# Kernel optimization log

Measured on AMD Instinct MI355X. Metric: run time of the kernel, lower is better.

Reference implementation:

```python
import jax, jax.numpy as jnp
import numpy as np
from jax import lax

DIM = 192
HEADS = 4
K = 3
PAD = 1


def conv2d(x, w, groups=1, pad=0):
    # x: [B,C,H,W], w: [O, C//groups, kh, kw]
    return lax.conv_general_dilated(
        x, w, window_strides=(1, 1), padding=[(pad, pad), (pad, pad)],
        dimension_numbers=("NCHW", "OIHW", "NCHW"), feature_group_count=groups)


def setup_inputs() -> dict:
    key = jax.random.key(0)
    ks = jax.random.split(key, 8)
    b, c, h, w = 2, DIM, 256, 256
    x = jax.random.normal(ks[0], (b, c, h, w), dtype=jnp.float32)
    y = jax.random.normal(ks[1], (b, c, h, w), dtype=jnp.float32)
    s = 0.05
    qk_w = jax.random.normal(ks[2], (2 * DIM, DIM, 1, 1), dtype=jnp.float32) * s
    qk_dw_w = jax.random.normal(ks[3], (2 * DIM, 1, K, K), dtype=jnp.float32) * s  # depthwise, groups=2*dim
    v_w = jax.random.normal(ks[4], (DIM, DIM, 1, 1), dtype=jnp.float32) * s
    v_dw_w = jax.random.normal(ks[5], (DIM, DIM, K, K), dtype=jnp.float32) * s    # NOTE: not grouped in source
    proj_w = jax.random.normal(ks[6], (DIM, DIM, 1, 1), dtype=jnp.float32) * s
    temperature = jnp.ones((HEADS, 1, 1), dtype=jnp.float32)
    return {"x": x, "y": y, "qk_w": qk_w, "qk_dw_w": qk_dw_w, "v_w": v_w,
            "v_dw_w": v_dw_w, "proj_w": proj_w, "temperature": temperature}


def reference(x, y, qk_w, qk_dw_w, v_w, v_dw_w, proj_w, temperature):
    b, c, h, w = x.shape
    hd = c // HEADS  # channels per head
    qk = conv2d(conv2d(x, qk_w), qk_dw_w, groups=2 * DIM, pad=PAD)  # [b, 2c, h, w]
    q, k = jnp.split(qk, 2, axis=1)
    v = conv2d(conv2d(y, v_w), v_dw_w, pad=PAD)  # full conv (groups=1), per source

    def to_heads(t):
        return t.reshape(b, HEADS, hd, h * w)  # b head c (hw)

    q, k, v = to_heads(q), to_heads(k), to_heads(v)
    # L2 normalize along spatial (last) axis, eps matches torch F.normalize (1e-12)
    q = q / jnp.maximum(jnp.linalg.norm(q, axis=-1, keepdims=True), 1e-12)
    k = k / jnp.maximum(jnp.linalg.norm(k, axis=-1, keepdims=True), 1e-12)
    attn = jnp.einsum("bhcn,bhdn->bhcd", q, k) * temperature  # [b, head, c, c]
    attn = jax.nn.softmax(attn, axis=-1)
    out = jnp.einsum("bhcd,bhdn->bhcn", attn, v)
    out = out.reshape(b, c, h, w)
    return conv2d(out, proj_w)
```

## Files before the change

### kernel.cpp

```cpp
#include <hip/hip_runtime.h>
#include <hip/hip_bf16.h>

#define NPIX 65536
#define CDIM 192
#define C2   384
#define HEADS 4
#define HD   48
#define PROW 258
#define XTROWS (PROW * PROW)

typedef float f32x4 __attribute__((ext_vector_type(4)));
typedef short short8 __attribute__((ext_vector_type(8)));

__device__ __forceinline__ unsigned short f2bf(float x) {
  union { float f; unsigned u; } v; v.f = x;
  unsigned r = v.u + 0x7fff + ((v.u >> 16) & 1);
  return (unsigned short)(r >> 16);
}
__device__ __forceinline__ float bf2f(unsigned short x) {
  union { unsigned u; float f; } v; v.u = ((unsigned)x) << 16;
  return v.f;
}
__device__ __forceinline__ int f4(int r) { return (r ^ (r >> 2)) & 3; }

__device__ __forceinline__ void gload_lds16(const void* g, void* l) {
  __builtin_amdgcn_global_load_lds(
      (const __attribute__((address_space(1))) unsigned int*)g,
      (__attribute__((address_space(3))) unsigned int*)l, 16, 0, 0);
}

__global__ __launch_bounds__(256) void castw_kernel(
    const float* __restrict__ qkw, const float* __restrict__ vw,
    unsigned short* __restrict__ wqk, unsigned short* __restrict__ wv) {
  int i = blockIdx.x * 256 + threadIdx.x;
  if (i < C2 * CDIM) wqk[i] = f2bf(qkw[i]);
  if (i < CDIM * CDIM) wv[i] = f2bf(vw[i]);
}

__global__ __launch_bounds__(512) void qk_mfma_kernel(
    const float* __restrict__ X, const unsigned short* __restrict__ W,
    unsigned short* __restrict__ Out) {
  const int px0 = blockIdx.x * 128;
  __shared__ __align__(16) short smem[17408];
  short* sA = smem;
  short* sB = smem + 12288;
  const int t = threadIdx.x;
  const int lane = t & 63;
  const int wid = t >> 6;
  const int cp = t & 15;
  const int pg = t >> 4;
  const int l15 = lane & 15;
  const int l4 = lane >> 4;

  f32x4 acc[3][8];
#pragma unroll
  for (int mi = 0; mi < 3; ++mi)
#pragma unroll
    for (int ni = 0; ni < 8; ++ni) acc[mi][ni] = (f32x4){0.f, 0.f, 0.f, 0.f};

  for (int k0 = 0; k0 < CDIM; k0 += 32) {
#pragma unroll
    for (int i = 0; i < 3; ++i) {
      int e = i * 512 + t;
      int oc = e >> 2, kg = e & 3;
      gload_lds16(W + (size_t)oc * CDIM + k0 + (kg ^ f4(oc)) * 8,
                  (char*)sA + ((size_t)i * 512 + (t & ~63)) * 16);
    }
    {
      const float* xp = X + (size_t)(k0 + 2 * cp) * NPIX + px0 + 4 * pg;
      float4 a = *(const float4*)xp;
      float4 b = *(const float4*)(xp + NPIX);
      float av[4] = {a.x, a.y, a.z, a.w};
      float bv[4] = {b.x, b.y, b.z, b.w};
#pragma unroll
      for (int i = 0; i < 4; ++i) {
        unsigned d = (unsigned)f2bf(av[i]) | ((unsigned)f2bf(bv[i]) << 16);
        *(unsigned*)&sB[(4 * pg + i) * 40 + 2 * cp] = d;
      }
    }
    asm volatile("s_waitcnt vmcnt(0)");
    __syncthreads();
    short8 af[3], bf[8];
#pragma unroll
    for (int mi = 0; mi < 3; ++mi) {
      int row = wid * 48 + mi * 16 + l15;
      af[mi] = *(const short8*)&sA[row * 32 + (l4 ^ f4(row)) * 8];
    }
#pragma unroll
    for (int ni = 0; ni < 8; ++ni)
      bf[ni] = *(const short8*)&sB[(ni * 16 + l15) * 40 + l4 * 8];
#pragma unroll
    for (int mi = 0; mi < 3; ++mi)
#pragma unroll
      for (int ni = 0; ni < 8; ++ni)
        acc[mi][ni] = __builtin_amdgcn_mfma_f32_16x16x32_bf16(
            af[mi], bf[ni], acc[mi][ni], 0, 0, 0);
    __syncthreads();
  }
  __syncthreads();
  short* zone = smem + wid * 2176;
#pragma unroll
  for (int mi = 0; mi < 3; ++mi) {
#pragma unroll
    for (int ni = 0; ni < 8; ++ni)
#pragma unroll
      for (int rg = 0; rg < 4; ++rg)
        zone[(l4 * 4 + rg) * 136 + ni * 16 + l15] =
            (short)f2bf(acc[mi][ni][rg]);
    asm volatile("s_waitcnt lgkmcnt(0)" ::: "memory");
    __builtin_amdgcn_sched_barrier(0);
#pragma unroll
    for (int it = 0; it < 4; ++it) {
      int e = it * 64 + lane;
      int ol = e >> 4, pxg = e & 15;
      short8 vv = *(const short8*)&zone[ol * 136 + pxg * 8];
      *(short8*)&Out[(size_t)(wid * 48 + mi * 16 + ol) * NPIX + px0 + pxg * 8] = vv;
    }
    asm volatile("s_waitcnt lgkmcnt(0)" ::: "memory");
    __builtin_amdgcn_sched_barrier(0);
  }
}

__global__ __launch_bounds__(256) void v_mfma_kernel(
    const float* __restrict__ Y, const unsigned short* __restrict__ W,
    unsigned short* __restrict__ Xt) {
  const int px0 = blockIdx.x * 64;
  const int h = px0 >> 8;
  const int w0 = px0 & 255;
  __shared__ short sX[64 * 40];
  __shared__ short sW[CDIM * 32];
  __shared__ short sZ[4 * 16 * 200];
  const int t = threadIdx.x;
  const int lane = t & 63;
  const int wid = t >> 6;
  const int cp = t & 15;
  const int pg = t >> 4;
  const int l15 = lane & 15;
  const int l4 = lane >> 4;

  f32x4 acc[12];
#pragma unroll
  for (int ni = 0; ni < 12; ++ni) acc[ni] = (f32x4){0.f, 0.f, 0.f, 0.f};

  for (int k0 = 0; k0 < CDIM; k0 += 32) {
#pragma unroll
    for (int i = 0; i < 3; ++i) {
      int e = i * 256 + t;
      int oc = e >> 2, kg = e & 3;
      gload_lds16(W + (size_t)oc * CDIM + k0 + (kg ^ f4(oc)) * 8,
                  (char*)sW + ((size_t)i * 256 + (t & ~63)) * 16);
    }
    {
      const float* xp = Y + (size_t)(k0 + 2 * cp) * NPIX + px0 + 4 * pg;
      float4 a = *(const float4*)xp;
      float4 b = *(const float4*)(xp + NPIX);
      float av[4] = {a.x, a.y, a.z, a.w};
      float bv[4] = {b.x, b.y, b.z, b.w};
#pragma unroll
      for (int i = 0; i < 4; ++i) {
        unsigned d = (unsigned)f2bf(av[i]) | ((unsigned)f2bf(bv[i]) << 16);
        *(unsigned*)&sX[(4 * pg + i) * 40 + 2 * cp] = d;
      }
    }
    asm volatile("s_waitcnt vmcnt(0)");
    __syncthreads();
    short8 af = *(const short8*)&sX[(wid * 16 + l15) * 40 + l4 * 8];
    short8 bf[12];
#pragma unroll
    for (int ni = 0; ni < 12; ++ni) {
      int row = ni * 16 + l15;
      bf[ni] = *(const short8*)&sW[row * 32 + (l4 ^ f4(row)) * 8];
    }
#pragma unroll
    for (int ni = 0; ni < 12; ++ni)
      acc[ni] = __builtin_amdgcn_mfma_f32_16x16x32_bf16(af, bf[ni], acc[ni],
                                                        0, 0, 0);
    __syncthreads();
  }
  short* zone = sZ + wid * (16 * 200);
#pragma unroll
  for (int ni = 0; ni < 12; ++ni)
#pragma unroll
    for (int rg = 0; rg < 4; ++rg)
      zone[(l4 * 4 + rg) * 200 + ni * 16 + l15] = (short)f2bf(acc[ni][rg]);
  asm volatile("s_waitcnt lgkmcnt(0)" ::: "memory");
  __builtin_amdgcn_sched_barrier(0);
#pragma unroll
  for (int it = 0; it < 6; ++it) {
    int e = it * 64 + lane;
    int pl = e / 24, cg = e % 24;
    short8 vv = *(const short8*)&zone[pl * 200 + cg * 8];
    size_t xrow = (size_t)(h + 1) * PROW + (w0 + wid * 16 + pl + 1);
    *(short8*)&Xt[xrow * CDIM + cg * 8] = vv;
  }
}

__global__ __launch_bounds__(128) void border_zero_kernel(
    unsigned short* __restrict__ Xt) {
  int pos = blockIdx.x;
  size_t row;
  if (pos < 258) row = pos;
  else if (pos < 516) row = (size_t)257 * PROW + (pos - 258);
  else { int i = pos - 516; row = (size_t)(1 + (i >> 1)) * PROW + ((i & 1) ? 257 : 0); }
  unsigned* p = (unsigned*)(Xt + row * CDIM);
  if (threadIdx.x < 96) p[threadIdx.x] = 0;
}

__global__ __launch_bounds__(256) void dwgram_kernel(
    const unsigned short* __restrict__ qkb, const float* __restrict__ dw,
    float* __restrict__ gpart_b, float* __restrict__ ssp_b) {
  const int head = blockIdx.y;
  const int blk = blockIdx.x;
  const int t = threadIdx.x;
  const int lane = t & 63;
  const int wid = t >> 6;

  __shared__ __align__(16) char smem[38400];
  short* zone = (short*)smem + wid * (96 * 40);

  const int qrow0 = HD * head, krow0 = CDIM + HD * head;
  const int p0 = (lane & 1) * 16;
  const int c0 = (lane >> 1) * 3;

  float wr[3][9];
#pragma unroll
  for (int j = 0; j < 3; ++j) {
    int ch = c0 + j;
    int srow = (ch < HD) ? (qrow0 + ch) : (krow0 + ch - HD);
#pragma unroll
    for (int i = 0; i < 9; ++i) wr[j][i] = dw[srow * 9 + i];
  }

  f32x4 acc[3][3];
#pragma unroll
  for (int mi = 0; mi < 3; ++mi)
#pragma unroll
    for (int nj = 0; nj < 3; ++nj) acc[mi][nj] = (f32x4){0.f, 0.f, 0.f, 0.f};
  float ss[3] = {0.f, 0.f, 0.f};

  const int pxbase = blk * 512 + wid * 128;
  for (int s = 0; s < 4; ++s) {
    const int px0 = pxbase + s * 32;
    const int hr = px0 >> 8;
    const int col0 = px0 & 255;
    const int cl = col0 + p0;
#pragma unroll
    for (int j = 0; j < 3; ++j) {
      int ch = c0 + j;
      int srow = (ch < HD) ? (qrow0 + ch) : (krow0 + ch - HD);
      const unsigned short* ip = qkb + (size_t)srow * NPIX;
      float win[3][18];
#pragma unroll
      for (int r = 0; r < 3; ++r) {
        int ir = hr - 1 + r;
        if ((unsigned)ir < 256u) {
          const unsigned short* rp = ip + ir * 256 + cl;
          short8 v0 = *(const short8*)rp;
          short8 v1 = *(const short8*)(rp + 8);
#pragma unroll
          for (int q = 0; q < 8; ++q) {
            win[r][1 + q] = bf2f((unsigned short)v0[q]);
            win[r][9 + q] = bf2f((unsigned short)v1[q]);
          }
          win[r][0]  = (cl > 0)        ? bf2f(rp[-1]) : 0.f;
          win[r][17] = (cl + 16 < 256) ? bf2f(rp[16]) : 0.f;
        } else {
#pragma unroll
          for (int q = 0; q < 18; ++q) win[r][q] = 0.f;
        }
      }
      unsigned pk[8];
#pragma unroll
      for (int p = 0; p < 16; ++p) {
        float sacc = 0.f;
#pragma unroll
        for (int r = 0; r < 3; ++r)
#pragma unroll
          for (int c = 0; c < 3; ++c) sacc += wr[j][r * 3 + c] * win[r][p + c];
        ss[j] += sacc * sacc;
        unsigned short bb = f2bf(sacc);
        if (p & 1) pk[p >> 1] |= ((unsigned)bb << 16);
        else       pk[p >> 1] = bb;
      }
      unsigned* zp = (unsigned*)&zone[ch * 40 + p0];
#pragma unroll
      for (int q = 0; q < 8; ++q) zp[q] = pk[q];
    }
    asm volatile("s_waitcnt lgkmcnt(0)" ::: "memory");
    __builtin_amdgcn_sched_barrier(0);
    short8 qf[3], kf[3];
#pragma unroll
    for (int mi = 0; mi < 3; ++mi)
      qf[mi] = *(const short8*)&zone[(mi * 16 + (lane & 15)) * 40 +
                                     (lane >> 4) * 8];
#pragma unroll
    for (int nj = 0; nj < 3; ++nj)
      kf[nj] = *(const short8*)&zone[(HD + nj * 16 + (lane & 15)) * 40 +
                                     (lane >> 4) * 8];
#pragma unroll
    for (int mi = 0; mi < 3; ++mi)
#pragma unroll
      for (int nj = 0; nj < 3; ++nj)
        acc[mi][nj] = __builtin_amdgcn_mfma_f32_16x16x32_bf16(
            qf[mi], kf[nj], acc[mi][nj], 0, 0, 0);
    asm volatile("s_waitcnt lgkmcnt(0)" ::: "memory");
    __builtin_amdgcn_sched_barrier(0);
  }
  __syncthreads();
  float* red   = (float*)smem;
  float* ssred = (float*)(smem + 36864);
#pragma unroll
  for (int mi = 0; mi < 3; ++mi)
#pragma unroll
    for (int nj = 0; nj < 3; ++nj) {
      int kj = nj * 16 + (lane & 15);
#pragma unroll
      for (int rg = 0; rg < 4; ++rg) {
        int qi = mi * 16 + (lane >> 4) * 4 + rg;
        red[wid * 2304 + qi * HD + kj] = acc[mi][nj][rg];
      }
    }
#pragma unroll
  for (int j = 0; j < 3; ++j) {
    float sj = ss[j] + __shfl_xor(ss[j], 1);
    if ((lane & 1) == 0) ssred[wid * 96 + c0 + j] = sj;
  }
  __syncthreads();
  float* gp = gpart_b + (size_t)(head * 128 + blk) * (HD * HD);
  for (int e = t; e < HD * HD; e += 256)
    gp[e] = red[e] + red[2304 + e] + red[4608 + e] + red[6912 + e];
  if (t < 96)
    ssp_b[(size_t)(head * 128 + blk) * 96 + t] =
        ssred[t] + ssred[96 + t] + ssred[192 + t] + ssred[288 + t];
}

__global__ __launch_bounds__(128) void normred_kernel(
    const float* __restrict__ ssp, float* __restrict__ norms) {
  int idx = blockIdx.x;
  int bh = idx / 96, ch = idx % 96;
  int l = threadIdx.x;
  float s = ssp[((size_t)bh * 128 + l) * 96 + ch];
#pragma unroll
  for (int off = 32; off; off >>= 1) s += __shfl_down(s, off);
  __shared__ float red[2];
  if ((l & 63) == 0) red[l >> 6] = s;
  __syncthreads();
  if (l == 0) {
    int b = bh >> 2, hh = bh & 3;
    int g = b * C2 + (ch < HD ? hh * HD + ch : CDIM + hh * HD + ch - HD);
    norms[g] = sqrtf(red[0] + red[1]);
  }
}

__global__ __launch_bounds__(256) void gramred_kernel(
    const float* __restrict__ part, float* __restrict__ logits) {
  int ij = blockIdx.x * 256 + threadIdx.x;
  int bh = blockIdx.y;
  if (ij >= HD * HD) return;
  const float* pp = part + (size_t)bh * 128 * (HD * HD);
  float s = 0.f;
  for (int sp = 0; sp < 128; ++sp) s += pp[(size_t)sp * (HD * HD) + ij];
  logits[(size_t)bh * (HD * HD) + ij] = s;
}

__global__ __launch_bounds__(64) void softmax_kernel(
    float* __restrict__ logits, const float* __restrict__ norms,
    const float* __restrict__ temperature) {
  int hh = blockIdx.x, b = blockIdx.y;
  int i = threadIdx.x;
  if (i >= HD) return;
  const float eps = 1e-12f;
  float temp = temperature[hh];
  float nq = fmaxf(norms[b * C2 + HD * hh + i], eps);
  float* row = logits + (((size_t)b * HEADS + hh) * HD + i) * HD;
  float vals[48];
  float mx = -1e30f;
#pragma unroll
  for (int j = 0; j < HD; ++j) {
    float nk = fmaxf(norms[b * C2 + CDIM + HD * hh + j], eps);
    float v = row[j] / (nq * nk) * temp;
    vals[j] = v;
    mx = fmaxf(mx, v);
  }
  float sum = 0.f;
#pragma unroll
  for (int j = 0; j < HD; ++j) {
    vals[j] = expf(vals[j] - mx);
    sum += vals[j];
  }
  float inv = 1.f / sum;
#pragma unroll
  for (int j = 0; j < HD; ++j) row[j] = vals[j] * inv;
}

__global__ __launch_bounds__(256) void buildM_kernel(
    const float* __restrict__ attn, const float* __restrict__ projw,
    float* __restrict__ M) {
  int idx = blockIdx.x * 256 + threadIdx.x;
  if (idx >= 2 * CDIM * CDIM) return;
  int d = idx % CDIM;
  int oc = (idx / CDIM) % CDIM;
  int b = idx / (CDIM * CDIM);
  int hh = d / HD, dd = d % HD;
  const float* arow = attn + ((size_t)b * HEADS + hh) * HD * HD;
  float s = 0.f;
#pragma unroll
  for (int c = 0; c < HD; ++c)
    s += projw[oc * CDIM + HD * hh + c] * arow[c * HD + dd];
  M[idx] = s;
}

__global__ __launch_bounds__(256) void wtrans_kernel(
    const float* __restrict__ M, const float* __restrict__ Wv,
    unsigned short* __restrict__ Wb) {
  const int ocb = blockIdx.x * 4;
  const int ec0 = blockIdx.y * 432;
  const int b = blockIdx.z;
  __shared__ float sM[4][CDIM];
  for (int i = threadIdx.x; i < 4 * CDIM; i += 256)
    sM[i / CDIM][i % CDIM] =
        M[((size_t)b * CDIM + ocb + i / CDIM) * CDIM + (i % CDIM)];
  __syncthreads();
  for (int e = ec0 + threadIdx.x; e < ec0 + 432; e += 256) {
    float a0 = 0.f, a1 = 0.f, a2 = 0.f, a3 = 0.f;
#pragma unroll 4
    for (int d = 0; d < CDIM; ++d) {
      float wv = Wv[(size_t)d * (CDIM * 9) + e];
      a0 += sM[0][d] * wv; a1 += sM[1][d] * wv;
      a2 += sM[2][d] * wv; a3 += sM[3][d] * wv;
    }
    int ic = e / 9, tap = e % 9;
    size_t base = (((size_t)b * 9 + tap) * CDIM) * CDIM + ic;
    Wb[base + (size_t)(ocb + 0) * CDIM] = f2bf(a0);
    Wb[base + (size_t)(ocb + 1) * CDIM] = f2bf(a1);
    Wb[base + (size_t)(ocb + 2) * CDIM] = f2bf(a2);
    Wb[base + (size_t)(ocb + 3) * CDIM] = f2bf(a3);
  }
}

__global__ __launch_bounds__(256) void conv3x3_mfma_kernel(
    const unsigned short* __restrict__ Xt,
    const unsigned short* __restrict__ Wb,
    float* __restrict__ out) {
  const int d = blockIdx.x;
  const int xcd = d & 7;
  const int j = d >> 3;
  const int h = xcd * 32 + j / 3;
  const int oc0 = (j % 3) * 64;

  __shared__ __align__(16) short sA[2][3 * 64 * 32];
  __shared__ __align__(16) short sB[2][260 * 32];

  const int t = threadIdx.x;
  const int lane = t & 63;
  const int wid = t >> 6;
  const int l15 = lane & 15;
  const int l4 = lane >> 4;

  f32x4 acc[4][4];
#pragma unroll
  for (int mi = 0; mi < 4; ++mi)
#pragma unroll
    for (int ni = 0; ni < 4; ++ni) acc[mi][ni] = (f32x4){0.f, 0.f, 0.f, 0.f};

#define STAGE(sidx, bi)                                                      \
  {                                                                          \
    const int r_ = (sidx) / 6;                                               \
    const int ic0_ = ((sidx) % 6) * 32;                                      \
    _Pragma("unroll")                                                        \
    for (int i = 0; i < 3; ++i) {                                            \
      int g = i * 256 + t;                                                   \
      int tap = g >> 8, e = g & 255, oc = e >> 2, ck = e & 3;                \
      gload_lds16(Wb + ((size_t)(r_ * 3 + tap) * CDIM + oc0 + oc) * CDIM +   \
                      ic0_ + (ck ^ f4(oc)) * 8,                              \
                  &sA[bi][(i * 256 + wid * 64) * 8]);                        \
    }                                                                        \
    const unsigned short* bsrc =                                             \
        Xt + (size_t)(h + r_) * PROW * CDIM + ic0_;                          \
    _Pragma("unroll")                                                        \
    for (int i = 0; i < 4; ++i) {                                            \
      int g = i * 256 + t;                                                   \
      int row = g >> 2, ck = g & 3;                                          \
      gload_lds16(bsrc + (size_t)row * CDIM + (ck ^ f4(row)) * 8,            \
                  &sB[bi][(i * 256 + wid * 64) * 8]);                        \
    }                                                                        \
    { int g = 1024 + wid * 2 + lane;                                         \
      int row = g >> 2, ck = g & 3;                                          \
      if (lane < 2)                                                          \
        gload_lds16(bsrc + (size_t)row * CDIM + (ck ^ f4(row)) * 8,          \
                    &sB[bi][(1024 + wid * 2) * 8]);                          \
    }                                                                        \
  }

  int cur = 0;
  STAGE(0, 0);
  for (int s = 0; s < 18; ++s) {
    if (s < 17) {
      STAGE(s + 1, cur ^ 1);
      asm volatile("s_waitcnt vmcnt(8)" ::: "memory");
    } else {
      asm volatile("s_waitcnt vmcnt(0)" ::: "memory");
    }
    __syncthreads();
#pragma unroll
    for (int c = 0; c < 3; ++c) {
      short8 af[4], bf[4];
#pragma unroll
      for (int mi = 0; mi < 4; ++mi) {
        int row = mi * 16 + l15;
        af[mi] = *(const short8*)&sA[cur][c * 2048 + row * 32 +
                                          (l4 ^ f4(row)) * 8];
      }
#pragma unroll
      for (int ni = 0; ni < 4; ++ni) {
        int row = wid * 64 + ni * 16 + l15 + c;
        bf[ni] = *(const short8*)&sB[cur][row * 32 + (l4 ^ f4(row)) * 8];
      }
#pragma unroll
      for (int mi = 0; mi < 4; ++mi)
#pragma unroll
        for (int ni = 0; ni < 4; ++ni)
          acc[mi][ni] = __builtin_amdgcn_mfma_f32_16x16x32_bf16(
              af[mi], bf[ni], acc[mi][ni], 0, 0, 0);
    }
    __syncthreads();
    cur ^= 1;
  }
#undef STAGE
#pragma unroll
  for (int mi = 0; mi < 4; ++mi) {
    int ocl = oc0 + mi * 16 + l4 * 4;
#pragma unroll
    for (int ni = 0; ni < 4; ++ni) {
      int wloc = wid * 64 + ni * 16 + l15;
#pragma unroll
      for (int rg = 0; rg < 4; ++rg)
        out[(size_t)(ocl + rg) * NPIX + h * 256 + wloc] = acc[mi][ni][rg];
    }
  }
}

extern "C" void kernel_launch(void* const* d_in, const int* in_sizes, int n_in,
                              void* d_out, int out_size, void* d_ws, size_t ws_size,
                              hipStream_t stream) {
  const float* x          = (const float*)d_in[0];
  const float* y          = (const float*)d_in[1];
  const float* qk_w       = (const float*)d_in[2];
  const float* qk_dw_w    = (const float*)d_in[3];
  const float* v_w        = (const float*)d_in[4];
  const float* v_dw_w     = (const float*)d_in[5];
  const float* proj_w     = (const float*)d_in[6];
  const float* temperature= (const float*)d_in[7];
  float* out = (float*)d_out;

  unsigned short* qkb = (unsigned short*)d_ws;
  unsigned short* Xt  = qkb;
  float* gpart  = (float*)(qkb + (size_t)C2 * NPIX);
  float* ssp    = gpart + (size_t)8 * 128 * HD * HD;
  float* norms  = ssp + (size_t)8 * 128 * 96;
  float* logits = norms + 768;
  float* M      = logits + 2 * HEADS * HD * HD;
  unsigned short* wqk = (unsigned short*)(M + 2 * CDIM * CDIM);
  unsigned short* wv  = wqk + C2 * CDIM;
  unsigned short* Wb  = wv + CDIM * CDIM;
  size_t needB = (size_t)((char*)(Wb + (size_t)2 * 9 * CDIM * CDIM) - (char*)d_ws);
  if (ws_size < needB) return;

  castw_kernel<<<dim3(288), dim3(256), 0, stream>>>(qk_w, v_w, wqk, wv);

  for (int b = 0; b < 2; ++b) {
    qk_mfma_kernel<<<dim3(512), dim3(512), 0, stream>>>(
        x + (size_t)b * CDIM * NPIX, wqk, qkb);
    dwgram_kernel<<<dim3(128, HEADS), dim3(256), 0, stream>>>(
        qkb, qk_dw_w,
        gpart + (size_t)b * HEADS * 128 * HD * HD,
        ssp + (size_t)b * HEADS * 128 * 96);
  }
  normred_kernel<<<dim3(768), dim3(128), 0, stream>>>(ssp, norms);
  gramred_kernel<<<dim3(9, 8), dim3(256), 0, stream>>>(gpart, logits);
  softmax_kernel<<<dim3(4, 2), dim3(64), 0, stream>>>(logits, norms, temperature);
  buildM_kernel<<<dim3(288), dim3(256), 0, stream>>>(logits, proj_w, M);
  wtrans_kernel<<<dim3(48, 4, 2), dim3(256), 0, stream>>>(M, v_dw_w, Wb);

  border_zero_kernel<<<dim3(1028), dim3(128), 0, stream>>>(Xt);
  for (int b = 0; b < 2; ++b) {
    v_mfma_kernel<<<dim3(1024), dim3(256), 0, stream>>>(
        y + (size_t)b * CDIM * NPIX, wv, Xt);
    conv3x3_mfma_kernel<<<dim3(768), dim3(256), 0, stream>>>(
        Xt, Wb + (size_t)b * 9 * CDIM * CDIM, out + (size_t)b * CDIM * NPIX);
  }
}
```

Before: 415.3 us.

## Batch v-path kernels over both images and load conv weights directly to registers

The v projection, border zeroing and 3x3 conv kernels now cover both batch images in a single launch via blockIdx.y, using a doubled padded workspace so the two batches no longer serialize. The conv kernel stops staging weight tiles through LDS and instead loads A fragments straight from global memory into registers each step, keeping only the activation tile double-buffered in shared memory. This lowers LDS usage and launch count, and gives a larger grid per launch. In exchange, weights are re-read from global or L2 by every block, and the loop now waits for all outstanding loads at the end of each step, which weakens the prefetch overlap.

```diff
diff --git a/kernel.cpp b/kernel.cpp
--- a/kernel.cpp
+++ b/kernel.cpp
@@ -122,8 +122,11 @@
 }
 
 __global__ __launch_bounds__(256) void v_mfma_kernel(
-    const float* __restrict__ Y, const unsigned short* __restrict__ W,
-    unsigned short* __restrict__ Xt) {
+    const float* __restrict__ Y0, const unsigned short* __restrict__ W,
+    unsigned short* __restrict__ Xt0) {
+  const int b = blockIdx.y;
+  const float* Y = Y0 + (size_t)b * CDIM * NPIX;
+  unsigned short* Xt = Xt0 + (size_t)b * XTROWS * CDIM;
   const int px0 = blockIdx.x * 64;
   const int h = px0 >> 8;
   const int w0 = px0 & 255;
@@ -153,9 +156,9 @@
     {
       const float* xp = Y + (size_t)(k0 + 2 * cp) * NPIX + px0 + 4 * pg;
       float4 a = *(const float4*)xp;
-      float4 b = *(const float4*)(xp + NPIX);
+      float4 b2 = *(const float4*)(xp + NPIX);
       float av[4] = {a.x, a.y, a.z, a.w};
-      float bv[4] = {b.x, b.y, b.z, b.w};
+      float bv[4] = {b2.x, b2.y, b2.z, b2.w};
 #pragma unroll
       for (int i = 0; i < 4; ++i) {
         unsigned d = (unsigned)f2bf(av[i]) | ((unsigned)f2bf(bv[i]) << 16);
@@ -196,7 +199,8 @@
 }
 
 __global__ __launch_bounds__(128) void border_zero_kernel(
-    unsigned short* __restrict__ Xt) {
+    unsigned short* __restrict__ Xt0) {
+  unsigned short* Xt = Xt0 + (size_t)blockIdx.y * XTROWS * CDIM;
   int pos = blockIdx.x;
   size_t row;
   if (pos < 258) row = pos;
@@ -439,16 +443,20 @@
 }
 
 __global__ __launch_bounds__(256) void conv3x3_mfma_kernel(
-    const unsigned short* __restrict__ Xt,
-    const unsigned short* __restrict__ Wb,
-    float* __restrict__ out) {
+    const unsigned short* __restrict__ XtAll,
+    const unsigned short* __restrict__ WbAll,
+    float* __restrict__ outAll) {
+  const int b = blockIdx.y;
+  const unsigned short* Xt = XtAll + (size_t)b * XTROWS * CDIM;
+  const unsigned short* Wb = WbAll + (size_t)b * 9 * CDIM * CDIM;
+  float* out = outAll + (size_t)b * CDIM * NPIX;
+
   const int d = blockIdx.x;
   const int xcd = d & 7;
   const int j = d >> 3;
   const int h = xcd * 32 + j / 3;
   const int oc0 = (j % 3) * 64;
 
-  __shared__ __align__(16) short sA[2][3 * 64 * 32];
   __shared__ __align__(16) short sB[2][260 * 32];
 
   const int t = threadIdx.x;
@@ -463,20 +471,12 @@
 #pragma unroll
     for (int ni = 0; ni < 4; ++ni) acc[mi][ni] = (f32x4){0.f, 0.f, 0.f, 0.f};
 
-#define STAGE(sidx, bi)                                                      \
+#define STAGE_B(sidx, bi)                                                    \
   {                                                                          \
-    const int r_ = (sidx) / 6;                                               \
-    const int ic0_ = ((sidx) % 6) * 32;                                      \
-    _Pragma("unroll")                                                        \
-    for (int i = 0; i < 3; ++i) {                                            \
-      int g = i * 256 + t;                                                   \
-      int tap = g >> 8, e = g & 255, oc = e >> 2, ck = e & 3;                \
-      gload_lds16(Wb + ((size_t)(r_ * 3 + tap) * CDIM + oc0 + oc) * CDIM +   \
-                      ic0_ + (ck ^ f4(oc)) * 8,                              \
-                  &sA[bi][(i * 256 + wid * 64) * 8]);                        \
-    }                                                                        \
+    const int rs_ = (sidx) / 6;                                              \
+    const int ics_ = ((sidx) % 6) * 32;                                      \
     const unsigned short* bsrc =                                             \
-        Xt + (size_t)(h + r_) * PROW * CDIM + ic0_;                          \
+        Xt + (size_t)(h + rs_) * PROW * CDIM + ics_;                         \
     _Pragma("unroll")                                                        \
     for (int i = 0; i < 4; ++i) {                                            \
       int g = i * 256 + t;                                                   \
@@ -492,41 +492,50 @@
     }                                                                        \
   }
 
+  STAGE_B(0, 0);
+  asm volatile("s_waitcnt vmcnt(0)" ::: "memory");
+  __syncthreads();
+
   int cur = 0;
-  STAGE(0, 0);
   for (int s = 0; s < 18; ++s) {
-    if (s < 17) {
-      STAGE(s + 1, cur ^ 1);
-      asm volatile("s_waitcnt vmcnt(8)" ::: "memory");
-    } else {
-      asm volatile("s_waitcnt vmcnt(0)" ::: "memory");
-    }
-    __syncthreads();
+    const int r_ = s / 6;
+    const int ic0_ = (s % 6) * 32;
+    short8 a0[4], a1[4], a2[4];
+    {
+      const unsigned short* abase =
+          Wb + ((size_t)(r_ * 3) * CDIM + oc0) * CDIM + ic0_;
+#pragma unroll
+      for (int mi = 0; mi < 4; ++mi) {
+        const unsigned short* p = abase + (size_t)(mi * 16 + l15) * CDIM + l4 * 8;
+        a0[mi] = *(const short8*)p;
+        a1[mi] = *(const short8*)(p + (size_t)CDIM * CDIM);
+        a2[mi] = *(const short8*)(p + (size_t)2 * CDIM * CDIM);
+      }
+    }
+    __builtin_amdgcn_sched_barrier(0);
+    if (s < 17) STAGE_B(s + 1, cur ^ 1);
 #pragma unroll
     for (int c = 0; c < 3; ++c) {
-      short8 af[4], bf[4];
-#pragma unroll
-      for (int mi = 0; mi < 4; ++mi) {
-        int row = mi * 16 + l15;
-        af[mi] = *(const short8*)&sA[cur][c * 2048 + row * 32 +
-                                          (l4 ^ f4(row)) * 8];
-      }
+      short8 bf[4];
 #pragma unroll
       for (int ni = 0; ni < 4; ++ni) {
         int row = wid * 64 + ni * 16 + l15 + c;
         bf[ni] = *(const short8*)&sB[cur][row * 32 + (l4 ^ f4(row)) * 8];
       }
 #pragma unroll
-      for (int mi = 0; mi < 4; ++mi)
+      for (int mi = 0; mi < 4; ++mi) {
+        short8 av = (c == 0) ? a0[mi] : (c == 1) ? a1[mi] : a2[mi];
 #pragma unroll
         for (int ni = 0; ni < 4; ++ni)
           acc[mi][ni] = __builtin_amdgcn_mfma_f32_16x16x32_bf16(
-              af[mi], bf[ni], acc[mi][ni], 0, 0, 0);
-    }
+              av, bf[ni], acc[mi][ni], 0, 0, 0);
+      }
+    }
+    asm volatile("s_waitcnt vmcnt(0)" ::: "memory");
     __syncthreads();
     cur ^= 1;
   }
-#undef STAGE
+#undef STAGE_B
 #pragma unroll
   for (int mi = 0; mi < 4; ++mi) {
     int ocl = oc0 + mi * 16 + l4 * 4;
@@ -553,9 +562,9 @@
   const float* temperature= (const float*)d_in[7];
   float* out = (float*)d_out;
 
-  unsigned short* qkb = (unsigned short*)d_ws;
-  unsigned short* Xt  = qkb;
-  float* gpart  = (float*)(qkb + (size_t)C2 * NPIX);
+  unsigned short* XtA = (unsigned short*)d_ws;
+  unsigned short* qkb = XtA;
+  float* gpart  = (float*)(XtA + (size_t)2 * XTROWS * CDIM);
   float* ssp    = gpart + (size_t)8 * 128 * HD * HD;
   float* norms  = ssp + (size_t)8 * 128 * 96;
   float* logits = norms + 768;
@@ -582,11 +591,7 @@
   buildM_kernel<<<dim3(288), dim3(256), 0, stream>>>(logits, proj_w, M);
   wtrans_kernel<<<dim3(48, 4, 2), dim3(256), 0, stream>>>(M, v_dw_w, Wb);
 
-  border_zero_kernel<<<dim3(1028), dim3(128), 0, stream>>>(Xt);
-  for (int b = 0; b < 2; ++b) {
-    v_mfma_kernel<<<dim3(1024), dim3(256), 0, stream>>>(
-        y + (size_t)b * CDIM * NPIX, wv, Xt);
-    conv3x3_mfma_kernel<<<dim3(768), dim3(256), 0, stream>>>(
-        Xt, Wb + (size_t)b * 9 * CDIM * CDIM, out + (size_t)b * CDIM * NPIX);
-  }
-}
+  border_zero_kernel<<<dim3(1028, 2), dim3(128), 0, stream>>>(XtA);
+  v_mfma_kernel<<<dim3(1024, 2), dim3(256), 0, stream>>>(y, wv, XtA);
+  conv3x3_mfma_kernel<<<dim3(768, 2), dim3(256), 0, stream>>>(XtA, Wb, out);
+}
```

Result: slower. 476.7 us (+14.8%).
